# Optimization experiments

Hardware: AMD Instinct MI355X
Metric: run time of the kernel (lower is better)

Reference implementation:

```python
import jax, jax.numpy as jnp
import numpy as np

DECAY = 0.99
EPS = 1e-6


def setup_inputs() -> dict:
    key = jax.random.key(0)
    k1, k2, k3, k4 = jax.random.split(key, 4)
    B, L, D, K = 32, 1024, 512, 8192
    return {
        "z_e": jax.random.normal(k1, (B, L, D), dtype=jnp.float32),
        "codebook": jax.random.normal(k2, (K, D), dtype=jnp.float32),
        "cluster_size": jax.random.uniform(k3, (K,), dtype=jnp.float32),
        "ema_w": jax.random.normal(k4, (K, D), dtype=jnp.float32),
    }


def reference(z_e, codebook, cluster_size, ema_w):
    B, L, D = z_e.shape
    K = codebook.shape[0]
    flat = z_e.reshape(-1, D)  # [N, D], N = B*L

    dist = ((flat * flat).sum(1, keepdims=True)
            - 2.0 * flat @ codebook.T
            + (codebook * codebook).sum(1))
    idx = jnp.argmin(dist, axis=1)  # [N]
    z_q = codebook[idx].reshape(B, L, D)

    # EMA statistics (training-mode buffer update); one-hot scatter -> segment_sum
    counts = jax.ops.segment_sum(jnp.ones((B * L,), flat.dtype), idx, num_segments=K)
    dw = jax.ops.segment_sum(flat, idx, num_segments=K)  # [K, D]
    new_cluster_size = DECAY * cluster_size + (1.0 - DECAY) * counts
    new_ema_w = DECAY * ema_w + (1.0 - DECAY) * dw
    n = new_cluster_size.sum()
    cs = (new_cluster_size + EPS) / (n + K * EPS) * n  # Laplace-smoothed counts
    new_codebook = new_ema_w / cs[:, None]

    # loss = mse(sg(z_q), z_e) + 0.25 * mse(z_e, sg(z_q)) = 1.25 * mse
    zq_sg = jax.lax.stop_gradient(z_q)
    loss = 1.25 * jnp.mean((z_e - zq_sg) ** 2)

    # straight-through estimator
    z_q_st = z_e + jax.lax.stop_gradient(z_q - z_e)
    return z_q_st, idx.reshape(B, L), loss, new_codebook, new_cluster_size, new_ema_w
```

## Files before the change

### kernel.cpp

```cpp
#include <hip/hip_runtime.h>


constexpr int N = 32768;
constexpr int D = 512;
constexpr int K = 8192;
constexpr int CAP  = 8192;
constexpr int CAPE = 4096;

constexpr float DECAYF  = 0.99f;
constexpr float OMDECAY = (float)(1.0 - 0.99);
constexpr float EPSF    = 1e-6f;
constexpr float KEPSF   = (float)(8192 * 1e-6);
constexpr float TAU1    = 1.0f;
constexpr float TAU2    = 0.02f;

typedef unsigned int       u32;
typedef unsigned short     u16;
typedef unsigned long long u64;
typedef float  f32x4 __attribute__((ext_vector_type(4)));
typedef u32    u32x4 __attribute__((ext_vector_type(4)));
typedef __bf16 bf16x8 __attribute__((ext_vector_type(8)));

#define AS1 __attribute__((address_space(1)))
#define AS3 __attribute__((address_space(3)))

constexpr size_t OFF_CNORM  = 0;
constexpr size_t OFF_IDX    = OFF_CNORM + K;
constexpr size_t OFF_CNTI   = OFF_IDX + N;
constexpr size_t OFF_FLAGC  = OFF_CNTI + K;
constexpr size_t OFF_FLAG2C = OFF_FLAGC + 1;
constexpr size_t OFF_NEXT   = OFF_FLAG2C + 1;
constexpr size_t OFF_OFFS   = OFF_NEXT + K;
constexpr size_t OFF_LIST   = OFF_OFFS + K + 1;
constexpr size_t OFF_FLAGL  = OFF_LIST + N;
constexpr size_t OFF_FLAG2L = OFF_FLAGL + CAP;
constexpr size_t OFF_PB1    = OFF_FLAG2L + N;
constexpr size_t OFF_PB2    = OFF_PB1 + 16 * CAP;
constexpr size_t OFF_PI1    = OFF_PB2 + 16 * CAP;
constexpr size_t OFF_ESLOT  = (OFF_PI1 + 16 * CAP + 1) & ~(size_t)1;
constexpr size_t OFF_SUMS   = (OFF_ESLOT + 2 * CAPE + 1) & ~(size_t)1;
constexpr size_t OFF_LOSSP  = (OFF_SUMS + 2 + 1) & ~(size_t)1;
constexpr size_t OFF_CBH    = (OFF_LOSSP + 2 * K + 3) & ~(size_t)3;
static_assert((OFF_ESLOT & 1) == 0 && (OFF_SUMS & 1) == 0 && (OFF_LOSSP & 1) == 0, "align");
static_assert((OFF_CBH & 3) == 0, "16B align for global_load_lds");

constexpr size_t OUT_ZQ   = 0;
constexpr size_t OUT_IDX  = OUT_ZQ + (size_t)N * D;
constexpr size_t OUT_LOSS = OUT_IDX + N;
constexpr size_t OUT_NCB  = OUT_LOSS + 1;
constexpr size_t OUT_NCS  = OUT_NCB + (size_t)K * D;
constexpr size_t OUT_EMA  = OUT_NCS + K;
constexpr size_t XH_F  = OUT_ZQ;
constexpr size_t PX2_F = OUT_ZQ + (size_t)N * 256;
constexpr size_t PB1H_F = OUT_EMA;
constexpr size_t PB2H_F = OUT_EMA + 4 * (size_t)N;
constexpr size_t PI1H_F = OUT_EMA + 8 * (size_t)N;

__device__ inline u16 f32_to_bf16_rne(float f)
{
    u32 u = __builtin_bit_cast(u32, f);
    u = (u + 0x7FFFu + ((u >> 16) & 1u)) >> 16;
    return (u16)u;
}

__global__ __launch_bounds__(256) void split_hi_kernel(const float* __restrict__ src,
                                                       u32x4* __restrict__ dst)
{
    const int T = blockIdx.x;
    const int w = threadIdx.x >> 6;
    const int l = threadIdx.x & 63;
    const int row = T * 16 + (l & 15);
#pragma unroll
    for (int i = 0; i < 4; ++i) {
        const int S  = w * 4 + i;
        const int q4 = S * 8 + (l >> 4) * 2;
        const float4 va = ((const float4*)src)[(size_t)row * 128 + q4];
        const float4 vb = ((const float4*)src)[(size_t)row * 128 + q4 + 1];
        const float a[8] = {va.x, va.y, va.z, va.w, vb.x, vb.y, vb.z, vb.w};
        u32x4 o;
#pragma unroll
        for (int j = 0; j < 4; ++j)
            ((u32*)&o)[j] = (u32)f32_to_bf16_rne(a[2 * j]) |
                            ((u32)f32_to_bf16_rne(a[2 * j + 1]) << 16);
        dst[((size_t)T * 16 + S) * 64 + l] = o;
    }
}

__global__ __launch_bounds__(256) void cbprep_kernel(const float* __restrict__ cb,
                                                     u32x4* __restrict__ CBH,
                                                     u32x4* __restrict__ CB2,
                                                     float* __restrict__ cnorm)
{
    const int T = blockIdx.x;
    const int w = threadIdx.x >> 6;
    const int l = threadIdx.x & 63;
    {
        const int row = T * 16 + (l & 15);
#pragma unroll
        for (int i = 0; i < 4; ++i) {
            const int S  = w * 4 + i;
            const int q4 = S * 8 + (l >> 4) * 2;
            const float4 va = ((const float4*)cb)[(size_t)row * 128 + q4];
            const float4 vb = ((const float4*)cb)[(size_t)row * 128 + q4 + 1];
            const float a[8] = {va.x, va.y, va.z, va.w, vb.x, vb.y, vb.z, vb.w};
            u32x4 o;
#pragma unroll
            for (int j = 0; j < 4; ++j)
                ((u32*)&o)[j] = (u32)f32_to_bf16_rne(a[2 * j]) |
                                ((u32)f32_to_bf16_rne(a[2 * j + 1]) << 16);
            CBH[((size_t)T * 16 + S) * 64 + l] = o;
        }
    }
    {
        const int row = T * 16 + (l & 15);
        const int cq  = l >> 4;
#pragma unroll
        for (int i = 0; i < 8; ++i) {
            const int S = w + 4 * i;
            const float4 v = ((const float4*)cb)[(size_t)row * 128 + S * 4 + cq];
            u32x4 o;
            const float a[4] = {v.x, v.y, v.z, v.w};
#pragma unroll
            for (int j = 0; j < 4; ++j) {
                const u16 hi = f32_to_bf16_rne(a[j]);
                const float hif = __builtin_bit_cast(float, (u32)hi << 16);
                const u16 lo = f32_to_bf16_rne(a[j] - hif);
                ((u32*)&o)[j] = (u32)hi | ((u32)lo << 16);
            }
            CB2[((size_t)T * 32 + S) * 64 + l] = o;
        }
    }
#pragma unroll
    for (int sub = 0; sub < 4; ++sub) {
        const int row = T * 16 + sub * 4 + w;
        const float4* r = (const float4*)(cb + (size_t)row * D);
        const float4 v0 = r[l];
        const float4 v1 = r[l + 64];
        float s = v0.x * v0.x + v0.y * v0.y + v0.z * v0.z + v0.w * v0.w
                + v1.x * v1.x + v1.y * v1.y + v1.z * v1.z + v1.w * v1.w;
#pragma unroll
        for (int m = 32; m >= 1; m >>= 1) s += __shfl_xor(s, m, 64);
        if (l == 0) cnorm[row] = s;
    }
}

__global__ __launch_bounds__(256) void repack_kernel(
    const float* __restrict__ z_e, const int* __restrict__ flag_cnt,
    const int* __restrict__ flag_list, u32x4* __restrict__ PX2)
{
    const int B = blockIdx.x;
    const int cnt = min(*flag_cnt, CAP);
    if (B * 16 >= cnt) return;
    const int w = threadIdx.x >> 6;
    const int l = threadIdx.x & 63;
    const int srow = B * 16 + (l & 15);
    const int n = (srow < cnt) ? (flag_list[srow] & (N - 1)) : 0;
    const int cq = l >> 4;
#pragma unroll
    for (int i = 0; i < 8; ++i) {
        const int S = w + 4 * i;
        const float4 v = ((const float4*)z_e)[(size_t)n * 128 + S * 4 + cq];
        u32x4 o;
        const float a[4] = {v.x, v.y, v.z, v.w};
#pragma unroll
        for (int j = 0; j < 4; ++j) {
            const u16 hi = f32_to_bf16_rne(a[j]);
            const float hif = __builtin_bit_cast(float, (u32)hi << 16);
            const u16 lo = f32_to_bf16_rne(a[j] - hif);
            ((u32*)&o)[j] = (u32)hi | ((u32)lo << 16);
        }
        PX2[((size_t)B * 32 + S) * 64 + l] = o;
    }
}

constexpr int BPH = 128, BCH = 128, KIH = 32;
constexpr int NSTEPH = 16;
constexpr int NCHQ   = 16;
constexpr int TOTQ   = NCHQ * NSTEPH;
constexpr int CELH = BCH * KIH;
constexpr int XELH = BPH * KIH;
constexpr int BUFH = CELH + XELH;

__global__ __launch_bounds__(256, 3) void argmin_hi_kernel(
    const u16* __restrict__ CBH, const u16* __restrict__ XH,
    const float* __restrict__ cnorm,
    float* __restrict__ pb1h, float* __restrict__ pb2h, int* __restrict__ pi1h)
{
    __shared__ __align__(16) u16 lds[2][BUFH];

    const int b    = blockIdx.x;
    const int kq   = (b & 7) >> 1;
    const int n0   = ((b >> 3) * 2 + (b & 1)) * BPH;
    const int tid  = threadIdx.x;
    const int w    = tid >> 6;
    const int lane = tid & 63;
    const int lhi  = lane >> 4;

    u32 cbo[2], xo[2];
#pragma unroll
    for (int m = 0; m < 2; ++m) {
        const int flat = m * 256 + tid;
        cbo[m] = (u32)(kq * 1048576 + (flat >> 6) * 8192 + (flat & 63) * 8);
        xo[m]  = (u32)((n0 / 16 + (flat >> 6)) * 8192 + (flat & 63) * 8);
    }

    auto stage = [&](int parity) {
        u16* bufp = &lds[parity][0];
#pragma unroll
        for (int m = 0; m < 2; ++m) {
            __builtin_amdgcn_global_load_lds((const AS1 u32*)(CBH + cbo[m]),
                (AS3 u32*)(bufp + (m * 256 + tid) * 8), 16, 0, 0);
            cbo[m] += 512;
            __builtin_amdgcn_global_load_lds((const AS1 u32*)(XH + xo[m]),
                (AS3 u32*)(bufp + CELH + (m * 256 + tid) * 8), 16, 0, 0);
            xo[m] += 512;
        }
    };

    float b1[8], b2[8]; int i1[8];
#pragma unroll
    for (int p = 0; p < 8; ++p) { b1[p] = INFINITY; b2[p] = INFINITY; i1[p] = 0; }

    stage(0);
    __syncthreads();
    int sc = 1;

    for (int cc = 0; cc < NCHQ; ++cc) {
        f32x4 acc[2][8];
        const f32x4 zero = {0.f, 0.f, 0.f, 0.f};
#pragma unroll
        for (int cg = 0; cg < 2; ++cg)
#pragma unroll
            for (int p = 0; p < 8; ++p) acc[cg][p] = zero;

        for (int s8 = 0; s8 < NSTEPH; ++s8) {
            const u16* cur = &lds[s8 & 1][0];
            if (sc < TOTQ) {
                if ((sc & (NSTEPH - 1)) == 0) {
#pragma unroll
                    for (int m = 0; m < 2; ++m) { cbo[m] += 65536 - 8192; xo[m] -= 8192; }
                }
                stage(sc & 1);
                ++sc;
            }
            u32x4 bfr[8];
#pragma unroll
            for (int p = 0; p < 8; ++p)
                bfr[p] = *(const u32x4*)(cur + CELH + p * 512 + lane * 8);
#pragma unroll
            for (int cg = 0; cg < 2; ++cg) {
                const u32x4 af = *(const u32x4*)(cur + (w * 2 + cg) * 512 + lane * 8);
#pragma unroll
                for (int p = 0; p < 8; ++p)
                    acc[cg][p] = __builtin_amdgcn_mfma_f32_16x16x32_bf16(
                        __builtin_bit_cast(bf16x8, af),
                        __builtin_bit_cast(bf16x8, bfr[p]), acc[cg][p], 0, 0, 0);
            }
            __syncthreads();
        }

        const int cb0 = (kq * NCHQ + cc) * BCH + w * 32;
#pragma unroll
        for (int cg = 0; cg < 2; ++cg) {
            const int code0 = cb0 + cg * 16 + lhi * 4;
            const float4 cn4 = *(const float4*)(cnorm + code0);
            const float cn[4] = {cn4.x, cn4.y, cn4.z, cn4.w};
#pragma unroll
            for (int p = 0; p < 8; ++p) {
                const f32x4 A = acc[cg][p];
                const float dv[4] = {cn[0] - 2.f * A.x, cn[1] - 2.f * A.y,
                                     cn[2] - 2.f * A.z, cn[3] - 2.f * A.w};
#pragma unroll
                for (int r = 0; r < 4; ++r) {
                    if (dv[r] < b1[p]) { b2[p] = b1[p]; b1[p] = dv[r]; i1[p] = code0 + r; }
                    else if (dv[r] < b2[p]) { b2[p] = dv[r]; }
                }
            }
        }
    }

#pragma unroll
    for (int p = 0; p < 8; ++p) {
#pragma unroll
        for (int m = 16; m <= 32; m <<= 1) {
            const float ob1 = __shfl_xor(b1[p], m, 64);
            const float ob2 = __shfl_xor(b2[p], m, 64);
            const int   oi1 = __shfl_xor(i1[p], m, 64);
            const float nb2 = fminf(fminf(b2[p], ob2), fmaxf(b1[p], ob1));
            if (ob1 < b1[p] || (ob1 == b1[p] && oi1 < i1[p])) { b1[p] = ob1; i1[p] = oi1; }
            b2[p] = nb2;
        }
    }

    __syncthreads();

    float* mb1 = (float*)&lds[0][0];
    float* mb2 = mb1 + 4 * BPH;
    int*   mi  = (int*)(mb2 + 4 * BPH);
    if (lane < 16) {
#pragma unroll
        for (int p = 0; p < 8; ++p) {
            const int pt = p * 16 + lane;
            mb1[w * BPH + pt] = b1[p];
            mb2[w * BPH + pt] = b2[p];
            mi [w * BPH + pt] = i1[p];
        }
    }
    __syncthreads();
    if (tid < BPH) {
        float fb1 = INFINITY, fb2 = INFINITY; int fi = 0;
        for (int ww = 0; ww < 4; ++ww) {
            const float a1 = mb1[ww * BPH + tid], a2 = mb2[ww * BPH + tid];
            const int   ai = mi[ww * BPH + tid];
            const float nb2 = fminf(fminf(fb2, a2), fmaxf(fb1, a1));
            if (a1 < fb1 || (a1 == fb1 && ai < fi)) { fb1 = a1; fi = ai; }
            fb2 = nb2;
        }
        const int n = n0 + tid;
        pb1h[kq * N + n] = fb1;
        pb2h[kq * N + n] = fb2;
        pi1h[kq * N + n] = fi;
    }
}

__global__ __launch_bounds__(256) void merge_hi_kernel(
    const float* __restrict__ pb1h, const float* __restrict__ pb2h,
    const int* __restrict__ pi1h,
    int* __restrict__ idx_i, float* __restrict__ idx_f,
    int* __restrict__ flag_cnt, int* __restrict__ flag_list,
    int* __restrict__ flag2_cnt, int* __restrict__ flag2_list)
{
    const int n = blockIdx.x * 256 + threadIdx.x;
    float fb1 = INFINITY, fb2 = INFINITY; int fi = 0x7fffffff;
#pragma unroll
    for (int q = 0; q < 4; ++q) {
        const float a1 = pb1h[q * N + n], a2 = pb2h[q * N + n];
        const int   ai = pi1h[q * N + n];
        const float nb2 = fminf(fminf(fb2, a2), fmaxf(fb1, a1));
        if (a1 < fb1 || (a1 == fb1 && ai < fi)) { fb1 = a1; fi = ai; }
        fb2 = nb2;
    }
    idx_i[n] = fi;
    idx_f[n] = (float)fi;
    if (fb2 - fb1 < TAU1) {
        const int pos = atomicAdd(flag_cnt, 1);
        if (pos < CAP) flag_list[pos] = n;
        else {
            const int p2 = atomicAdd(flag2_cnt, 1);
            if ((unsigned)p2 < (unsigned)N) flag2_list[p2] = n;
        }
    }
}

constexpr int CEL2 = 512 * 32;
constexpr int XEL2 = 128 * 32;
constexpr int BUF2 = CEL2 + XEL2;

__global__ __launch_bounds__(512, 2) void argmin_part_kernel(
    const u16* __restrict__ CB2, const u16* __restrict__ PX2,
    const float* __restrict__ cnorm, const int* __restrict__ flag_cnt,
    float* __restrict__ pb1, float* __restrict__ pb2, int* __restrict__ pi1)
{
    const int q  = blockIdx.x & 15;
    const int sb = blockIdx.x >> 4;
    const int cnt = min(*flag_cnt, CAP);
    if (sb * 128 >= cnt) return;
    const int n0s = sb * 128;

    __shared__ __align__(16) u16 lds[2][BUF2];

    const int tid  = threadIdx.x;
    const int w    = tid >> 6;
    const int lane = tid & 63;
    const int lhi  = lane >> 4;

    auto stage = [&](u16* bufp, int s) {
#pragma unroll
        for (int j = 0; j < 4; ++j) {
            const int slot = j * 512 + tid;
            const u16* gsrc = CB2 + (((size_t)(q * 32 + (slot >> 6)) * 32 + s) * 512
                                     + (slot & 63) * 8);
            __builtin_amdgcn_global_load_lds((const AS1 u32*)gsrc,
                                             (AS3 u32*)(bufp + slot * 8), 16, 0, 0);
        }
        const u16* gx = PX2 + (((size_t)(n0s / 16 + (tid >> 6)) * 32 + s) * 512
                               + (tid & 63) * 8);
        __builtin_amdgcn_global_load_lds((const AS1 u32*)gx,
                                         (AS3 u32*)(bufp + CEL2 + tid * 8), 16, 0, 0);
    };

    float b1[8], b2[8]; int i1[8];
#pragma unroll
    for (int p = 0; p < 8; ++p) { b1[p] = INFINITY; b2[p] = INFINITY; i1[p] = 0; }

    f32x4 acc[4][8];
    const f32x4 zero = {0.f, 0.f, 0.f, 0.f};
#pragma unroll
    for (int cg = 0; cg < 4; ++cg)
#pragma unroll
        for (int p = 0; p < 8; ++p) acc[cg][p] = zero;

    stage(&lds[0][0], 0);
    __syncthreads();

#pragma unroll 2
    for (int s = 0; s < 32; ++s) {
        const u16* cur = (s & 1) ? &lds[1][0] : &lds[0][0];
        u16* nxt       = (s & 1) ? &lds[0][0] : &lds[1][0];
        if (s + 1 < 32) stage(nxt, s + 1);

        u32x4 bfr[8];
#pragma unroll
        for (int p = 0; p < 8; ++p)
            bfr[p] = *(const u32x4*)(cur + CEL2 + p * 512 + lane * 8);
#pragma unroll
        for (int cg = 0; cg < 4; ++cg) {
            const u32x4 af = *(const u32x4*)(cur + (w * 4 + cg) * 512 + lane * 8);
            u32x4 as;
            as.x = (af.x >> 16) | (af.x << 16);
            as.y = (af.y >> 16) | (af.y << 16);
            as.z = (af.z >> 16) | (af.z << 16);
            as.w = (af.w >> 16) | (af.w << 16);
#pragma unroll
            for (int p = 0; p < 8; ++p) {
                acc[cg][p] = __builtin_amdgcn_mfma_f32_16x16x32_bf16(
                    __builtin_bit_cast(bf16x8, af), __builtin_bit_cast(bf16x8, bfr[p]),
                    acc[cg][p], 0, 0, 0);
                acc[cg][p] = __builtin_amdgcn_mfma_f32_16x16x32_bf16(
                    __builtin_bit_cast(bf16x8, as), __builtin_bit_cast(bf16x8, bfr[p]),
                    acc[cg][p], 0, 0, 0);
            }
        }
        __syncthreads();
    }

    const int cb0 = q * 512 + w * 64;
#pragma unroll
    for (int cg = 0; cg < 4; ++cg) {
        const int code0 = cb0 + cg * 16 + lhi * 4;
        const float4 cn4 = *(const float4*)(cnorm + code0);
        const float cn[4] = {cn4.x, cn4.y, cn4.z, cn4.w};
#pragma unroll
        for (int p = 0; p < 8; ++p) {
            const f32x4 A = acc[cg][p];
            const float dv[4] = {cn[0] - 2.f * A.x, cn[1] - 2.f * A.y,
                                 cn[2] - 2.f * A.z, cn[3] - 2.f * A.w};
#pragma unroll
            for (int r = 0; r < 4; ++r) {
                if (dv[r] < b1[p]) { b2[p] = b1[p]; b1[p] = dv[r]; i1[p] = code0 + r; }
                else if (dv[r] < b2[p]) { b2[p] = dv[r]; }
            }
        }
    }

#pragma unroll
    for (int p = 0; p < 8; ++p) {
#pragma unroll
        for (int m = 16; m <= 32; m <<= 1) {
            const float ob1 = __shfl_xor(b1[p], m, 64);
            const float ob2 = __shfl_xor(b2[p], m, 64);
            const int   oi1 = __shfl_xor(i1[p], m, 64);
            const float nb2 = fminf(fminf(b2[p], ob2), fmaxf(b1[p], ob1));
            if (ob1 < b1[p] || (ob1 == b1[p] && oi1 < i1[p])) { b1[p] = ob1; i1[p] = oi1; }
            b2[p] = nb2;
        }
    }

    __syncthreads();

    float* mb1 = (float*)&lds[0][0];
    float* mb2 = mb1 + 8 * 128;
    int*   mi  = (int*)(mb2 + 8 * 128);
    if (lane < 16) {
#pragma unroll
        for (int p = 0; p < 8; ++p) {
            const int pt = p * 16 + lane;
            mb1[w * 128 + pt] = b1[p];
            mb2[w * 128 + pt] = b2[p];
            mi [w * 128 + pt] = i1[p];
        }
    }
    __syncthreads();
    if (tid < 128) {
        float fb1 = INFINITY, fb2 = INFINITY; int fi = 0;
        for (int ww = 0; ww < 8; ++ww) {
            const float a1 = mb1[ww * 128 + tid], a2 = mb2[ww * 128 + tid];
            const int   ai = mi[ww * 128 + tid];
            const float nb2 = fminf(fminf(fb2, a2), fmaxf(fb1, a1));
            if (a1 < fb1 || (a1 == fb1 && ai < fi)) { fb1 = a1; fi = ai; }
            fb2 = nb2;
        }
        const int slot = n0s + tid;
        pb1[q * CAP + slot] = fb1;
        pb2[q * CAP + slot] = fb2;
        pi1[q * CAP + slot] = fi;
    }
}

__global__ __launch_bounds__(256) void combine_kernel(
    const int* __restrict__ flag_cnt, const int* __restrict__ flag_list,
    const float* __restrict__ pb1, const float* __restrict__ pb2,
    const int* __restrict__ pi1,
    int* __restrict__ idx_i, float* __restrict__ idx_f,
    int* __restrict__ flag2_cnt, int* __restrict__ flag2_list)
{
    const int s = blockIdx.x * 256 + threadIdx.x;
    const int cnt = min(*flag_cnt, CAP);
    if (s >= cnt) return;
    float fb1 = INFINITY, fb2 = INFINITY; int fi = 0x7fffffff;
#pragma unroll
    for (int q = 0; q < 16; ++q) {
        const float a1 = pb1[q * CAP + s], a2 = pb2[q * CAP + s];
        const int   ai = pi1[q * CAP + s];
        const float nb2 = fminf(fminf(fb2, a2), fmaxf(fb1, a1));
        if (a1 < fb1 || (a1 == fb1 && ai < fi)) { fb1 = a1; fi = ai; }
        fb2 = nb2;
    }
    const int n = flag_list[s] & (N - 1);
    idx_i[n] = fi;
    idx_f[n] = (float)fi;
    if (fb2 - fb1 < TAU2) {
        const int p2 = atomicAdd(flag2_cnt, 1);
        if ((unsigned)p2 < (unsigned)N) flag2_list[p2] = n;
    }
}

__global__ __launch_bounds__(256) void exact_part_kernel(
    const float* __restrict__ x, const float* __restrict__ cb,
    const float* __restrict__ cnorm, const int* __restrict__ flag2_cnt,
    const int* __restrict__ flag2_list, u64* __restrict__ eslot)
{
    __shared__ float4 xs[128];
    __shared__ u64 red[256];
    const int cnt = min(*flag2_cnt, CAPE);
    const int nwork = cnt * 16;
    for (int j = blockIdx.x; j < nwork; j += gridDim.x) {
        const int s = j >> 4;
        const int q = j & 15;
        const int n = flag2_list[s] & (N - 1);
        __syncthreads();
        if (threadIdx.x < 128)
            xs[threadIdx.x] = ((const float4*)(x + (size_t)n * D))[threadIdx.x];
        __syncthreads();
        u64 bestp = ~0ull;
#pragma unroll
        for (int c = 0; c < 2; ++c) {
            const int k = q * 512 + c * 256 + threadIdx.x;
            const float4* crow = (const float4*)(cb + (size_t)k * D);
            float a0 = 0.f, a1 = 0.f, a2 = 0.f, a3 = 0.f;
            for (int d = 0; d < 128; ++d) {
                const float4 xv = xs[d], cv = crow[d];
                a0 = fmaf(xv.x, cv.x, a0);
                a1 = fmaf(xv.y, cv.y, a1);
                a2 = fmaf(xv.z, cv.z, a2);
                a3 = fmaf(xv.w, cv.w, a3);
            }
            const float dist = cnorm[k] - 2.0f * ((a0 + a1) + (a2 + a3));
            u32 ub = __builtin_bit_cast(u32, dist);
            ub = (ub & 0x80000000u) ? ~ub : (ub | 0x80000000u);
            const u64 pk = ((u64)ub << 32) | (u32)k;
            bestp = bestp < pk ? bestp : pk;
        }
        red[threadIdx.x] = bestp;
        __syncthreads();
        for (int off = 128; off > 0; off >>= 1) {
            if (threadIdx.x < off) {
                const u64 o = red[threadIdx.x + off];
                if (o < red[threadIdx.x]) red[threadIdx.x] = o;
            }
            __syncthreads();
        }
        if (threadIdx.x == 0) atomicMin(&eslot[s], red[0]);
    }
}

__global__ __launch_bounds__(256) void exact_write_kernel(
    const int* __restrict__ flag2_cnt, const int* __restrict__ flag2_list,
    const u64* __restrict__ eslot, int* __restrict__ idx_i, float* __restrict__ idx_f)
{
    const int s = blockIdx.x * 256 + threadIdx.x;
    const int cnt = min(*flag2_cnt, CAPE);
    if (s >= cnt) return;
    const int n = flag2_list[s] & (N - 1);
    const int k = (int)(eslot[s] & (u64)(K - 1));
    idx_i[n] = k;
    idx_f[n] = (float)k;
}

__global__ __launch_bounds__(256) void count_kernel(
    const int* __restrict__ idx_i, int* __restrict__ cnti)
{
    const int p = blockIdx.x * 256 + threadIdx.x;
    atomicAdd(&cnti[idx_i[p] & (K - 1)], 1);
}

__global__ __launch_bounds__(256) void scan_kernel(
    const int* __restrict__ cnti, const float* __restrict__ csz,
    int* __restrict__ offs, int* __restrict__ nxt,
    float* __restrict__ ncs, double* __restrict__ n_sum)
{
    __shared__ int    tsum[256];
    __shared__ double dsum[256];
    const int t = threadIdx.x;
    const int base = t * 32;
    int s = 0;
    double dn = 0.0;
#pragma unroll
    for (int i = 0; i < 32; ++i) {
        const int c = cnti[base + i];
        s += c;
        const float v = DECAYF * csz[base + i] + OMDECAY * (float)c;
        ncs[base + i] = v;
        dn += (double)v;
    }
    tsum[t] = s; dsum[t] = dn;
    __syncthreads();
    int run = 0;
    for (int j = 0; j < t; ++j) run += tsum[j];
#pragma unroll
    for (int i = 0; i < 32; ++i) {
        offs[base + i] = run;
        nxt[base + i] = run;
        run += cnti[base + i];
    }
    if (t == 255) offs[K] = run;
    if (t == 0) {
        double tot = 0.0;
        for (int j = 0; j < 256; ++j) tot += dsum[j];
        n_sum[0] = tot;
    }
}

__global__ __launch_bounds__(256) void fill_kernel(
    const int* __restrict__ idx_i, int* __restrict__ nxt, int* __restrict__ list)
{
    const int p = blockIdx.x * 256 + threadIdx.x;
    const int k = idx_i[p] & (K - 1);
    const int pos = atomicAdd(&nxt[k], 1);
    if ((unsigned)pos < (unsigned)N) list[pos] = p;
}

__global__ __launch_bounds__(128) void gather_finalize_kernel(
    const float* __restrict__ x, const float* __restrict__ cb,
    const int* __restrict__ offs, const int* __restrict__ list,
    const float* __restrict__ ema_w, const float* __restrict__ ncs,
    const double* __restrict__ n_sum, float* __restrict__ new_ema,
    float* __restrict__ new_cb, float* __restrict__ zq,
    double* __restrict__ loss_part)
{
    const int k = blockIdx.x;
    const int t = threadIdx.x;
    const int beg = min(offs[k], N), end = min(offs[k + 1], N);
    const size_t o = (size_t)k * 128 + t;
    const float4 c = ((const float4*)cb)[o];
    float4 acc = {0.f, 0.f, 0.f, 0.f};
    float lsum = 0.f;
    for (int i = beg; i < end; ++i) {
        const int p = list[i] & (N - 1);
        const float4 v = ((const float4*)x)[(size_t)p * 128 + t];
        acc.x += v.x; acc.y += v.y; acc.z += v.z; acc.w += v.w;
        ((float4*)zq)[(size_t)p * 128 + t] = c;
        const float d0 = v.x - c.x, d1 = v.y - c.y, d2 = v.z - c.z, d3 = v.w - c.w;
        lsum += d0 * d0 + d1 * d1 + d2 * d2 + d3 * d3;
    }
    const float n = (float)n_sum[0];
    const float csm = (ncs[k] + EPSF) / (n + KEPSF) * n;
    const float4 e = ((const float4*)ema_w)[o];
    float4 ne;
    ne.x = DECAYF * e.x + OMDECAY * acc.x;
    ne.y = DECAYF * e.y + OMDECAY * acc.y;
    ne.z = DECAYF * e.z + OMDECAY * acc.z;
    ne.w = DECAYF * e.w + OMDECAY * acc.w;
    ((float4*)new_ema)[o] = ne;
    float4 nc;
    nc.x = ne.x / csm; nc.y = ne.y / csm; nc.z = ne.z / csm; nc.w = ne.w / csm;
    ((float4*)new_cb)[o] = nc;

#pragma unroll
    for (int m = 32; m >= 1; m >>= 1) lsum += __shfl_xor(lsum, m, 64);
    __shared__ float prt[2];
    if ((t & 63) == 0) prt[t >> 6] = lsum;
    __syncthreads();
    if (t == 0) loss_part[k] = (double)(prt[0] + prt[1]);
}

__global__ __launch_bounds__(256) void loss_reduce_kernel(
    const double* __restrict__ loss_part, float* __restrict__ out_loss)
{
    __shared__ double red[256];
    const int t = threadIdx.x;
    double s = 0.0;
    for (int i = t; i < K; i += 256) s += loss_part[i];
    red[t] = s;
    __syncthreads();
    for (int off = 128; off > 0; off >>= 1) {
        if (t < off) red[t] += red[t + off];
        __syncthreads();
    }
    if (t == 0)
        out_loss[0] = (float)(1.25 * (red[0] / (double)((size_t)N * D)));
}

extern "C" void kernel_launch(void* const* d_in, const int* in_sizes, int n_in,
                              void* d_out, int out_size, void* d_ws, size_t ws_size,
                              hipStream_t stream)
{
    const float* z_e   = (const float*)d_in[0];
    const float* cbook = (const float*)d_in[1];
    const float* csz   = (const float*)d_in[2];
    const float* ema_w = (const float*)d_in[3];

    float* out = (float*)d_out;
    u32*   ws  = (u32*)d_ws;

    float*  cnorm      = (float*)(ws + OFF_CNORM);
    int*    idx_i      = (int*)(ws + OFF_IDX);
    int*    cnti       = (int*)(ws + OFF_CNTI);
    int*    flag_cnt   = (int*)(ws + OFF_FLAGC);
    int*    flag2_cnt  = (int*)(ws + OFF_FLAG2C);
    int*    nxt        = (int*)(ws + OFF_NEXT);
    int*    offs       = (int*)(ws + OFF_OFFS);
    int*    list       = (int*)(ws + OFF_LIST);
    int*    flag_list  = (int*)(ws + OFF_FLAGL);
    int*    flag2_list = (int*)(ws + OFF_FLAG2L);
    float*  pb1        = (float*)(ws + OFF_PB1);
    float*  pb2        = (float*)(ws + OFF_PB2);
    int*    pi1        = (int*)(ws + OFF_PI1);
    u64*    eslot      = (u64*)(ws + OFF_ESLOT);
    double* n_sum      = (double*)(ws + OFF_SUMS);
    double* loss_part  = (double*)(ws + OFF_LOSSP);
    u16*    CBH        = (u16*)(ws + OFF_CBH);

    u16* XH  = (u16*)(out + XH_F);
    u16* PX2 = (u16*)(out + PX2_F);
    u16* CB2 = (u16*)(out + OUT_NCB);
    float* pb1h = out + PB1H_F;
    float* pb2h = out + PB2H_F;
    int*   pi1h = (int*)(out + PI1H_F);

    hipMemsetAsync(ws + OFF_CNTI, 0, (K + 2) * sizeof(u32), stream);
    hipMemsetAsync(ws + OFF_ESLOT, 0xFF, CAPE * sizeof(u64), stream);

    split_hi_kernel<<<N / 16, 256, 0, stream>>>(z_e, (u32x4*)XH);
    cbprep_kernel<<<K / 16, 256, 0, stream>>>(cbook, (u32x4*)CBH, (u32x4*)CB2, cnorm);

    argmin_hi_kernel<<<(N / BPH) * 4, 256, 0, stream>>>(CBH, XH, cnorm,
                                                        pb1h, pb2h, pi1h);

    merge_hi_kernel<<<N / 256, 256, 0, stream>>>(pb1h, pb2h, pi1h, idx_i,
                                                 out + OUT_IDX, flag_cnt, flag_list,
                                                 flag2_cnt, flag2_list);

    repack_kernel<<<CAP / 16, 256, 0, stream>>>(z_e, flag_cnt, flag_list, (u32x4*)PX2);

    argmin_part_kernel<<<(CAP / 128) * 16, 512, 0, stream>>>(CB2, PX2, cnorm, flag_cnt,
                                                             pb1, pb2, pi1);

    combine_kernel<<<CAP / 256, 256, 0, stream>>>(flag_cnt, flag_list, pb1, pb2, pi1,
                                                  idx_i, out + OUT_IDX,
                                                  flag2_cnt, flag2_list);

    exact_part_kernel<<<2048, 256, 0, stream>>>(z_e, cbook, cnorm, flag2_cnt,
                                                flag2_list, eslot);

    exact_write_kernel<<<CAPE / 256, 256, 0, stream>>>(flag2_cnt, flag2_list, eslot,
                                                       idx_i, out + OUT_IDX);

    count_kernel<<<N / 256, 256, 0, stream>>>(idx_i, cnti);

    scan_kernel<<<1, 256, 0, stream>>>(cnti, csz, offs, nxt, out + OUT_NCS, n_sum);

    fill_kernel<<<N / 256, 256, 0, stream>>>(idx_i, nxt, list);

    gather_finalize_kernel<<<K, 128, 0, stream>>>(z_e, cbook, offs, list, ema_w,
                                                  out + OUT_NCS, n_sum,
                                                  out + OUT_EMA, out + OUT_NCB,
                                                  out + OUT_ZQ, loss_part);

    loss_reduce_kernel<<<1, 256, 0, stream>>>(loss_part, out + OUT_LOSS);
}
```

Baseline: 899.4 us.

## Replace LDS double-buffered staging with direct global loads in argmin MFMA kernel

```diff
diff --git a/kernel.cpp b/kernel.cpp
--- a/kernel.cpp
+++ b/kernel.cpp
@@ -42,7 +42,7 @@
 constexpr size_t OFF_LOSSP  = (OFF_SUMS + 2 + 1) & ~(size_t)1;
 constexpr size_t OFF_CBH    = (OFF_LOSSP + 2 * K + 3) & ~(size_t)3;
 static_assert((OFF_ESLOT & 1) == 0 && (OFF_SUMS & 1) == 0 && (OFF_LOSSP & 1) == 0, "align");
-static_assert((OFF_CBH & 3) == 0, "16B align for global_load_lds");
+static_assert((OFF_CBH & 3) == 0, "16B align");
 
 constexpr size_t OUT_ZQ   = 0;
 constexpr size_t OUT_IDX  = OUT_ZQ + (size_t)N * D;
@@ -173,20 +173,16 @@
     }
 }
 
-constexpr int BPH = 128, BCH = 128, KIH = 32;
-constexpr int NSTEPH = 16;
-constexpr int NCHQ   = 16;
-constexpr int TOTQ   = NCHQ * NSTEPH;
-constexpr int CELH = BCH * KIH;
-constexpr int XELH = BPH * KIH;
-constexpr int BUFH = CELH + XELH;
-
-__global__ __launch_bounds__(256, 3) void argmin_hi_kernel(
+constexpr int BPH = 128;
+
+__global__ __launch_bounds__(256, 2) void argmin_hi_kernel(
     const u16* __restrict__ CBH, const u16* __restrict__ XH,
     const float* __restrict__ cnorm,
     float* __restrict__ pb1h, float* __restrict__ pb2h, int* __restrict__ pi1h)
 {
-    __shared__ __align__(16) u16 lds[2][BUFH];
+    __shared__ float mb1[4 * BPH];
+    __shared__ float mb2[4 * BPH];
+    __shared__ int   mi [4 * BPH];
 
     const int b    = blockIdx.x;
     const int kq   = (b & 7) >> 1;
@@ -196,72 +192,42 @@
     const int lane = tid & 63;
     const int lhi  = lane >> 4;
 
-    u32 cbo[2], xo[2];
-#pragma unroll
-    for (int m = 0; m < 2; ++m) {
-        const int flat = m * 256 + tid;
-        cbo[m] = (u32)(kq * 1048576 + (flat >> 6) * 8192 + (flat & 63) * 8);
-        xo[m]  = (u32)((n0 / 16 + (flat >> 6)) * 8192 + (flat & 63) * 8);
-    }
-
-    auto stage = [&](int parity) {
-        u16* bufp = &lds[parity][0];
-#pragma unroll
-        for (int m = 0; m < 2; ++m) {
-            __builtin_amdgcn_global_load_lds((const AS1 u32*)(CBH + cbo[m]),
-                (AS3 u32*)(bufp + (m * 256 + tid) * 8), 16, 0, 0);
-            cbo[m] += 512;
-            __builtin_amdgcn_global_load_lds((const AS1 u32*)(XH + xo[m]),
-                (AS3 u32*)(bufp + CELH + (m * 256 + tid) * 8), 16, 0, 0);
-            xo[m] += 512;
-        }
-    };
+    const u16* cbase = CBH + ((size_t)(kq * 128 + w * 32) * 8192) + lane * 8;
+    const u16* xbase = XH + ((size_t)(n0 / 16) * 8192) + lane * 8;
 
     float b1[8], b2[8]; int i1[8];
 #pragma unroll
     for (int p = 0; p < 8; ++p) { b1[p] = INFINITY; b2[p] = INFINITY; i1[p] = 0; }
 
-    stage(0);
-    __syncthreads();
-    int sc = 1;
-
-    for (int cc = 0; cc < NCHQ; ++cc) {
-        f32x4 acc[2][8];
+    for (int c = 0; c < 8; ++c) {
+        f32x4 acc[4][8];
         const f32x4 zero = {0.f, 0.f, 0.f, 0.f};
 #pragma unroll
-        for (int cg = 0; cg < 2; ++cg)
+        for (int cg = 0; cg < 4; ++cg)
 #pragma unroll
             for (int p = 0; p < 8; ++p) acc[cg][p] = zero;
 
-        for (int s8 = 0; s8 < NSTEPH; ++s8) {
-            const u16* cur = &lds[s8 & 1][0];
-            if (sc < TOTQ) {
-                if ((sc & (NSTEPH - 1)) == 0) {
-#pragma unroll
-                    for (int m = 0; m < 2; ++m) { cbo[m] += 65536 - 8192; xo[m] -= 8192; }
-                }
-                stage(sc & 1);
-                ++sc;
-            }
-            u32x4 bfr[8];
+#pragma unroll 2
+        for (int s = 0; s < 16; ++s) {
+            u32x4 af[4], bfr[8];
+#pragma unroll
+            for (int cg = 0; cg < 4; ++cg)
+                af[cg] = *(const u32x4*)(cbase + ((c * 4 + cg) * 16 + s) * 512);
 #pragma unroll
             for (int p = 0; p < 8; ++p)
-                bfr[p] = *(const u32x4*)(cur + CELH + p * 512 + lane * 8);
-#pragma unroll
-            for (int cg = 0; cg < 2; ++cg) {
-                const u32x4 af = *(const u32x4*)(cur + (w * 2 + cg) * 512 + lane * 8);
+                bfr[p] = *(const u32x4*)(xbase + (p * 16 + s) * 512);
+#pragma unroll
+            for (int cg = 0; cg < 4; ++cg)
 #pragma unroll
                 for (int p = 0; p < 8; ++p)
                     acc[cg][p] = __builtin_amdgcn_mfma_f32_16x16x32_bf16(
-                        __builtin_bit_cast(bf16x8, af),
+                        __builtin_bit_cast(bf16x8, af[cg]),
                         __builtin_bit_cast(bf16x8, bfr[p]), acc[cg][p], 0, 0, 0);
-            }
-            __syncthreads();
-        }
-
-        const int cb0 = (kq * NCHQ + cc) * BCH + w * 32;
-#pragma unroll
-        for (int cg = 0; cg < 2; ++cg) {
+        }
+
+        const int cb0 = kq * 2048 + w * 512 + c * 64;
+#pragma unroll
+        for (int cg = 0; cg < 4; ++cg) {
             const int code0 = cb0 + cg * 16 + lhi * 4;
             const float4 cn4 = *(const float4*)(cnorm + code0);
             const float cn[4] = {cn4.x, cn4.y, cn4.z, cn4.w};
@@ -292,11 +258,6 @@
         }
     }
 
-    __syncthreads();
-
-    float* mb1 = (float*)&lds[0][0];
-    float* mb2 = mb1 + 4 * BPH;
-    int*   mi  = (int*)(mb2 + 4 * BPH);
     if (lane < 16) {
 #pragma unroll
         for (int p = 0; p < 8; ++p) {
```

New measurement: 856.0 us. 1.05x faster.
